# Kernel tuning notes

Measured on AMD Instinct MI355X. Metric: run time of the kernel, lower is better.

Reference implementation:

```python
import jax, jax.numpy as jnp
import numpy as np
from jax import lax

LOOKBACK = 336
N_FEATURES = 164
HORIZON = 96
D_MODEL = 64
D_STATE = 16
D_CONV = 4
EXPAND = 2
D_INNER = EXPAND * D_MODEL  # 128
DT_RANK = (D_MODEL + 15) // 16  # 4
MLP_HIDDEN = 64
BATCH = 512


def setup_inputs() -> dict:
    key = jax.random.key(0)
    ks = jax.random.split(key, 20)
    f32 = jnp.float32
    inp = {}
    inp["x_raw"] = jax.random.normal(ks[0], (BATCH, LOOKBACK), f32)
    inp["x_features"] = jax.random.normal(ks[1], (BATCH, N_FEATURES), f32)
    # embed Linear(1, d_model)
    inp["embed_W"] = jax.random.normal(ks[2], (1, D_MODEL), f32) * 0.5
    inp["embed_b"] = jnp.zeros((D_MODEL,), f32)
    # Mamba params (mamba-ssm layout, stored as [in, out] for matmul)
    inp["in_W"] = jax.random.normal(ks[3], (D_MODEL, 2 * D_INNER), f32) * (1.0 / np.sqrt(D_MODEL))
    inp["conv_W"] = jax.random.normal(ks[4], (D_INNER, D_CONV), f32) * 0.3
    inp["conv_b"] = jnp.zeros((D_INNER,), f32)
    inp["xproj_W"] = jax.random.normal(ks[5], (D_INNER, DT_RANK + 2 * D_STATE), f32) * (1.0 / np.sqrt(D_INNER))
    inp["dt_W"] = jax.random.normal(ks[6], (DT_RANK, D_INNER), f32) * (1.0 / np.sqrt(DT_RANK))
    inp["dt_b"] = jax.random.uniform(ks[7], (D_INNER,), f32, -4.0, -2.0)  # softplus -> small dt
    # A_log init = log(arange(1..d_state)) broadcast over d_inner, as in mamba-ssm
    inp["A_log"] = jnp.log(jnp.broadcast_to(jnp.arange(1, D_STATE + 1, dtype=f32), (D_INNER, D_STATE)))
    inp["D"] = jnp.ones((D_INNER,), f32)
    inp["out_W"] = jax.random.normal(ks[8], (D_INNER, D_MODEL), f32) * (1.0 / np.sqrt(D_INNER))
    # MLP stream
    inp["mlp_W1"] = jax.random.normal(ks[9], (N_FEATURES, MLP_HIDDEN), f32) * (1.0 / np.sqrt(N_FEATURES))
    inp["mlp_b1"] = jnp.zeros((MLP_HIDDEN,), f32)
    inp["mlp_W2"] = jax.random.normal(ks[10], (MLP_HIDDEN, MLP_HIDDEN // 2), f32) * (1.0 / np.sqrt(MLP_HIDDEN))
    inp["mlp_b2"] = jnp.zeros((MLP_HIDDEN // 2,), f32)
    # prediction head
    fin = D_MODEL + MLP_HIDDEN // 2
    inp["head_W"] = jax.random.normal(ks[11], (fin, HORIZON), f32) * (1.0 / np.sqrt(fin))
    inp["head_b"] = jnp.zeros((HORIZON,), f32)
    return inp


def silu(x):
    return x * jax.nn.sigmoid(x)


def mamba_block(u, in_W, conv_W, conv_b, xproj_W, dt_W, dt_b, A_log, D, out_W):
    # u: [B, L, d_model]
    B_, L, _ = u.shape
    xz = u @ in_W                      # [B, L, 2*D_INNER]
    x, z = jnp.split(xz, 2, axis=-1)   # each [B, L, D_INNER]
    # causal depthwise conv1d (pad left d_conv-1), then SiLU
    xc = x.transpose(0, 2, 1)          # [B, D_INNER, L]
    kern = conv_W[:, None, :]          # [D_INNER, 1, K] (OIH)
    xc = lax.conv_general_dilated(xc, kern, window_strides=(1,),
                                  padding=[(D_CONV - 1, 0)],
                                  dimension_numbers=("NCH", "OIH", "NCH"),
                                  feature_group_count=D_INNER)
    xc = silu(xc + conv_b[None, :, None])
    x = xc.transpose(0, 2, 1)          # [B, L, D_INNER]
    # input-dependent SSM params
    x_dbl = x @ xproj_W                # [B, L, DT_RANK + 2*D_STATE]
    dt = x_dbl[..., :DT_RANK]
    Bm = x_dbl[..., DT_RANK:DT_RANK + D_STATE]          # [B, L, N]
    Cm = x_dbl[..., DT_RANK + D_STATE:]                 # [B, L, N]
    delta = jax.nn.softplus(dt @ dt_W + dt_b)           # [B, L, D_INNER]
    A = -jnp.exp(A_log)                                 # [D_INNER, N]

    # selective scan over time
    def step(h, inps):
        d_t, B_t, C_t, x_t = inps  # [B,Di], [B,N], [B,N], [B,Di]
        dA = jnp.exp(d_t[:, :, None] * A[None])              # [B, Di, N]
        dBx = (d_t * x_t)[:, :, None] * B_t[:, None, :]      # [B, Di, N]
        h = dA * h + dBx
        y_t = jnp.einsum("bdn,bn->bd", h, C_t)
        return h, y_t

    h0 = jnp.zeros((B_, D_INNER, D_STATE), u.dtype)
    seq = (delta.transpose(1, 0, 2), Bm.transpose(1, 0, 2),
           Cm.transpose(1, 0, 2), x.transpose(1, 0, 2))
    _, ys = lax.scan(step, h0, seq)        # ys: [L, B, D_INNER]
    y = ys.transpose(1, 0, 2) + x * D[None, None, :]
    y = y * silu(z)
    return y @ out_W                        # [B, L, d_model]


def reference(x_raw, x_features, embed_W, embed_b, in_W, conv_W, conv_b,
              xproj_W, dt_W, dt_b, A_log, D, out_W,
              mlp_W1, mlp_b1, mlp_W2, mlp_b2, head_W, head_b):
    # embed raw series: [B, L] -> [B, L, 1] -> [B, L, d_model]
    h = x_raw[..., None] @ embed_W + embed_b
    h = mamba_block(h, in_W, conv_W, conv_b, xproj_W, dt_W, dt_b, A_log, D, out_W)
    h_mamba_out = h[:, -1, :]                       # [B, d_model]
    h_mlp = jax.nn.relu(x_features @ mlp_W1 + mlp_b1) @ mlp_W2 + mlp_b2
    h_final = jnp.concatenate([h_mamba_out, h_mlp], axis=1)
    return h_final @ head_W + head_b                # [B, horizon]
```

## Files before the change

kernel.cpp:

```cpp
#include <hip/hip_runtime.h>
#include <math.h>

#define LOOKBACK 336
#define NFEAT    164
#define HORIZON  96
#define DMODEL   64
#define DSTATE   16
#define DINNER   128
#define MLPH     64
#define BATCH    512
#define XCP      132
#define NG       4
#define GSEG     84
#define CHK      12
#define NCH      7
#define HSTR     20

typedef float v2f __attribute__((ext_vector_type(2)));

__device__ __forceinline__ float fast_rcp(float x) { return __builtin_amdgcn_rcpf(x); }
__device__ __forceinline__ float silu_f(float x) {
    return x * fast_rcp(1.f + __expf(-x));
}

__global__ __launch_bounds__(512, 2) void mamba_one(
    const float* __restrict__ x_raw,   const float* __restrict__ x_features,
    const float* __restrict__ embed_W, const float* __restrict__ embed_b,
    const float* __restrict__ in_W,
    const float* __restrict__ conv_W,  const float* __restrict__ conv_b,
    const float* __restrict__ xproj_W, const float* __restrict__ dt_W,
    const float* __restrict__ dt_b,    const float* __restrict__ A_log,
    const float* __restrict__ Dvec,    const float* __restrict__ out_W,
    const float* __restrict__ mlp_W1,  const float* __restrict__ mlp_b1,
    const float* __restrict__ mlp_W2,  const float* __restrict__ mlp_b2,
    const float* __restrict__ head_W,  const float* __restrict__ head_b,
    float* __restrict__ out)
{
    __shared__ __align__(16) float xrl[344];
    __shared__ __align__(16) float xprojT[20*XCP];
    __shared__ __align__(16) float xcbuf[2][NG][CHK*XCP];
    __shared__ __align__(16) float Bsh[NG][CHK][DSTATE];
    __shared__ __align__(16) float dtraw[NG][CHK][4];
    __shared__ float xcl[DINNER], zsil[DINNER], Cl[DSTATE], yv[DINNER];
    __shared__ float hfin[96], mlph[MLPH];

    const int tid = threadIdx.x;
    const int b   = blockIdx.x;
    const int g   = tid >> 7;
    const int ch  = tid & 127;

    for (int i = tid; i < 339; i += 512)
        xrl[i] = (i >= 3) ? x_raw[b*LOOKBACK + i - 3] : 0.f;
    for (int idx = tid; idx < 20*DINNER; idx += 512) {
        int jj = idx >> 7, d = idx & 127;
        xprojT[jj*XCP + d] = xproj_W[d*36 + jj];
    }

    float w1 = 0.f, w0 = 0.f;
    for (int dm = 0; dm < DMODEL; ++dm) {
        float w = in_W[dm*(2*DINNER) + ch];
        w1 = fmaf(embed_W[dm], w, w1);
        w0 = fmaf(embed_b[dm], w, w0);
    }
    const float4 cw = *(const float4*)&conv_W[ch*4];
    const float  cb = conv_b[ch];
    const float dtw0 = dt_W[ch],       dtw1 = dt_W[128 + ch],
                dtw2 = dt_W[256 + ch], dtw3 = dt_W[384 + ch];
    const float dtb_r = dt_b[ch];
    bool structured = true;
    #pragma unroll
    for (int i = 0; i < 16; ++i) {
        float a = __expf(A_log[ch*DSTATE + i]);
        float ex = (float)(i + 1);
        structured = structured && (fabsf(a - ex) < 1e-3f * ex);
    }
    const bool sfast = __all(structured);
    __syncthreads();

    {
        float* xw = &xcbuf[0][g][0];
        const float* xr = &xrl[g*GSEG];
        if (g == 0) {
            for (int tt = 0; tt < CHK; ++tt) {
                float acc = cb;
                if (tt >= 3) acc = fmaf(fmaf(xr[tt],   w1, w0), cw.x, acc);
                if (tt >= 2) acc = fmaf(fmaf(xr[tt+1], w1, w0), cw.y, acc);
                if (tt >= 1) acc = fmaf(fmaf(xr[tt+2], w1, w0), cw.z, acc);
                acc = fmaf(fmaf(xr[tt+3], w1, w0), cw.w, acc);
                xw[tt*XCP + ch] = silu_f(acc);
            }
        } else {
            float e0 = fmaf(xr[0], w1, w0);
            float e1 = fmaf(xr[1], w1, w0);
            float e2 = fmaf(xr[2], w1, w0);
            #pragma unroll
            for (int tt = 0; tt < CHK; ++tt) {
                float e3 = fmaf(xr[tt+3], w1, w0);
                float acc = cb + e0*cw.x + e1*cw.y + e2*cw.z + e3*cw.w;
                xw[tt*XCP + ch] = silu_f(acc);
                e0 = e1; e1 = e2; e2 = e3;
            }
        }
    }
    __syncthreads();

    v2f h01={0,0},h23={0,0},h45={0,0},h67={0,0},
        h89={0,0},hAB={0,0},hCD={0,0},hEF={0,0};
    float dacc = 0.f;

    for (int c = 0; c < NCH; ++c) {
        const int buf = c & 1;

        if (ch < 120) {
            const int tt = ch / 10;
            const int j0 = (ch - tt*10) * 2;
            const float* p0   = &xprojT[j0*XCP];
            const float* p1   = &xprojT[(j0+1)*XCP];
            const float* xrow = &xcbuf[buf][g][tt*XCP];
            v2f a0 = {0,0}, a1 = {0,0};
            #pragma unroll 8
            for (int d = 0; d < DINNER; d += 4) {
                float4 xv = *(const float4*)(xrow + d);
                float4 q0 = *(const float4*)(p0 + d);
                float4 q1 = *(const float4*)(p1 + d);
                v2f xl = {xv.x, xv.y}, xh = {xv.z, xv.w};
                v2f q0l = {q0.x, q0.y}, q0h = {q0.z, q0.w};
                v2f q1l = {q1.x, q1.y}, q1h = {q1.z, q1.w};
                a0 = __builtin_elementwise_fma(xl, q0l, a0);
                a0 = __builtin_elementwise_fma(xh, q0h, a0);
                a1 = __builtin_elementwise_fma(xl, q1l, a1);
                a1 = __builtin_elementwise_fma(xh, q1h, a1);
            }
            float r0 = a0.x + a0.y, r1 = a1.x + a1.y;
            if (j0 < 4) *(float2*)&dtraw[g][tt][j0] = make_float2(r0, r1);
            else        *(float2*)&Bsh[g][tt][j0-4] = make_float2(r0, r1);
        }
        __syncthreads();

        const float* xs = &xcbuf[buf][g][0];
        if (__builtin_expect(sfast, 1)) {
            #pragma unroll
            for (int tt = 0; tt < CHK; ++tt) {
                float4 dr = *(const float4*)&dtraw[g][tt][0];
                float dv = fmaf(dr.x, dtw0, fmaf(dr.y, dtw1,
                           fmaf(dr.z, dtw2, fmaf(dr.w, dtw3, dtb_r))));
                float e  = __expf(dv);
                float p  = 1.f + e;
                float r  = fast_rcp(p);
                float dl = (dv > 80.f) ? dv : __logf(p);
                dacc += dl;
                float ux = dl * xs[tt*XCP + ch];
                float4 B0 = *(const float4*)&Bsh[g][tt][0];
                float4 B1 = *(const float4*)&Bsh[g][tt][4];
                float4 B2 = *(const float4*)&Bsh[g][tt][8];
                float4 B3 = *(const float4*)&Bsh[g][tt][12];
                float r2 = r*r;
                v2f r2v = {r2, r2};
                v2f p01 = {r, r2};
                v2f p23 = p01*r2v, p45 = p23*r2v, p67 = p45*r2v, p89 = p67*r2v,
                    pAB = p89*r2v, pCD = pAB*r2v, pEF = pCD*r2v;
                v2f uxv = {ux, ux};
                h01 = __builtin_elementwise_fma(p01, h01, uxv*(v2f){B0.x,B0.y});
                h23 = __builtin_elementwise_fma(p23, h23, uxv*(v2f){B0.z,B0.w});
                h45 = __builtin_elementwise_fma(p45, h45, uxv*(v2f){B1.x,B1.y});
                h67 = __builtin_elementwise_fma(p67, h67, uxv*(v2f){B1.z,B1.w});
                h89 = __builtin_elementwise_fma(p89, h89, uxv*(v2f){B2.x,B2.y});
                hAB = __builtin_elementwise_fma(pAB, hAB, uxv*(v2f){B2.z,B2.w});
                hCD = __builtin_elementwise_fma(pCD, hCD, uxv*(v2f){B3.x,B3.y});
                hEF = __builtin_elementwise_fma(pEF, hEF, uxv*(v2f){B3.z,B3.w});
            }
        } else {
            const float* Arow = A_log + ch*DSTATE;
            for (int tt = 0; tt < CHK; ++tt) {
                float4 dr = *(const float4*)&dtraw[g][tt][0];
                float dv = fmaf(dr.x, dtw0, fmaf(dr.y, dtw1,
                           fmaf(dr.z, dtw2, fmaf(dr.w, dtw3, dtb_r))));
                float e  = __expf(dv);
                float dl = (dv > 15.f) ? dv : __logf(1.f + e);
                dacc += dl;
                float ux = dl * xs[tt*XCP + ch];
                const float* Brow = &Bsh[g][tt][0];
                float hv[16] = {h01.x,h01.y,h23.x,h23.y,h45.x,h45.y,h67.x,h67.y,
                                h89.x,h89.y,hAB.x,hAB.y,hCD.x,hCD.y,hEF.x,hEF.y};
                for (int i = 0; i < 16; ++i)
                    hv[i] = fmaf(__expf(-__expf(Arow[i])*dl), hv[i], ux*Brow[i]);
                h01=(v2f){hv[0],hv[1]};   h23=(v2f){hv[2],hv[3]};
                h45=(v2f){hv[4],hv[5]};   h67=(v2f){hv[6],hv[7]};
                h89=(v2f){hv[8],hv[9]};   hAB=(v2f){hv[10],hv[11]};
                hCD=(v2f){hv[12],hv[13]}; hEF=(v2f){hv[14],hv[15]};
            }
        }

        if (c + 1 < NCH) {
            float* xw = &xcbuf[buf^1][g][0];
            const float* xr = &xrl[g*GSEG + (c+1)*CHK];
            float e0 = fmaf(xr[0], w1, w0);
            float e1 = fmaf(xr[1], w1, w0);
            float e2 = fmaf(xr[2], w1, w0);
            float v = 0.f;
            #pragma unroll
            for (int tt = 0; tt < CHK; ++tt) {
                float e3 = fmaf(xr[tt+3], w1, w0);
                float acc = cb + e0*cw.x + e1*cw.y + e2*cw.z + e3*cw.w;
                v = silu_f(acc);
                xw[tt*XCP + ch] = v;
                e0 = e1; e1 = e2; e2 = e3;
            }
            if (g == NG-1 && c + 1 == NCH-1) xcl[ch] = v;
        }
        __syncthreads();
    }

    float* hpart = &xcbuf[0][0][0];
    float* dsum  = &Bsh[0][0][0];
    {
        float4* hp = (float4*)&hpart[(g*128 + ch)*HSTR];
        hp[0] = make_float4(h01.x,h01.y,h23.x,h23.y);
        hp[1] = make_float4(h45.x,h45.y,h67.x,h67.y);
        hp[2] = make_float4(h89.x,h89.y,hAB.x,hAB.y);
        hp[3] = make_float4(hCD.x,hCD.y,hEF.x,hEF.y);
        dsum[g*128 + ch] = dacc;
    }
    __syncthreads();

    float H[16];
    if (tid < 128) {
        {
            const float4* hp = (const float4*)&hpart[tid*HSTR];
            float4 a = hp[0], bq = hp[1], cq = hp[2], dq = hp[3];
            H[0]=a.x;  H[1]=a.y;  H[2]=a.z;  H[3]=a.w;
            H[4]=bq.x; H[5]=bq.y; H[6]=bq.z; H[7]=bq.w;
            H[8]=cq.x; H[9]=cq.y; H[10]=cq.z;H[11]=cq.w;
            H[12]=dq.x;H[13]=dq.y;H[14]=dq.z;H[15]=dq.w;
        }
        for (int gg = 1; gg < NG; ++gg) {
            float D = dsum[gg*128 + tid];
            const float4* hp = (const float4*)&hpart[(gg*128 + tid)*HSTR];
            float4 a = hp[0], bq = hp[1], cq = hp[2], dq = hp[3];
            float hg[16] = {a.x,a.y,a.z,a.w,bq.x,bq.y,bq.z,bq.w,
                            cq.x,cq.y,cq.z,cq.w,dq.x,dq.y,dq.z,dq.w};
            if (structured) {
                float r = __expf(-D);
                float pw = 1.f;
                #pragma unroll
                for (int i = 0; i < 16; ++i) {
                    pw *= r;
                    H[i] = fmaf(pw, H[i], hg[i]);
                }
            } else {
                #pragma unroll
                for (int i = 0; i < 16; ++i)
                    H[i] = fmaf(__expf(-__expf(A_log[tid*DSTATE+i])*D), H[i], hg[i]);
            }
        }
    } else if (tid < 256) {
        const int c2 = tid - 128;
        float a1 = 0.f, a0 = 0.f;
        for (int dm = 0; dm < DMODEL; ++dm) {
            float w = in_W[dm*(2*DINNER) + DINNER + c2];
            a1 = fmaf(embed_W[dm], w, a1);
            a0 = fmaf(embed_b[dm], w, a0);
        }
        float zv = fmaf(xrl[338], a1, a0);
        zsil[c2] = silu_f(zv);
    } else if (tid < 320) {
        const int lane = tid - 256;
        const int n = lane & 15, q = lane >> 4;
        float acc = 0.f;
        for (int d = q*32; d < q*32 + 32; ++d)
            acc = fmaf(xcl[d], xproj_W[d*36 + 20 + n], acc);
        acc += __shfl_xor(acc, 16);
        acc += __shfl_xor(acc, 32);
        if (lane < 16) Cl[n] = acc;
    } else if (tid >= 384) {
        const int lane = tid - 384;
        const int j = lane >> 1, k = lane & 1;
        const float* xf = x_features + b*NFEAT;
        float acc = 0.f;
        const int f0 = k*82, f1 = (k ? NFEAT : 82);
        for (int f = f0; f < f1; ++f)
            acc = fmaf(xf[f], mlp_W1[f*MLPH + j], acc);
        acc += __shfl_xor(acc, 1);
        if (k == 0) mlph[j] = fmaxf(acc + mlp_b1[j], 0.f);
    }
    __syncthreads();

    if (tid < 128) {
        float acc = 0.f;
        #pragma unroll
        for (int i = 0; i < 16; ++i) acc = fmaf(H[i], Cl[i], acc);
        float y = acc + xcl[tid]*Dvec[tid];
        yv[tid] = y * zsil[tid];
    } else if (tid < 192) {
        const int lane = tid - 128;
        const int j = lane >> 1, k = lane & 1;
        float acc = 0.f;
        for (int kk = k*32; kk < k*32 + 32; ++kk)
            acc = fmaf(mlph[kk], mlp_W2[kk*32 + j], acc);
        acc += __shfl_xor(acc, 1);
        if (k == 0) hfin[64 + j] = acc + mlp_b2[j];
    }
    __syncthreads();

    if (tid < 256) {
        const int o = tid >> 2, k = tid & 3;
        float acc = 0.f;
        for (int d = k*32; d < k*32 + 32; ++d)
            acc = fmaf(yv[d], out_W[d*DMODEL + o], acc);
        acc += __shfl_xor(acc, 1);
        acc += __shfl_xor(acc, 2);
        if (k == 0) hfin[o] = acc;
    }
    __syncthreads();

    if (tid < 192) {
        const int o = tid >> 1, k = tid & 1;
        float acc = 0.f;
        for (int i = k*48; i < k*48 + 48; ++i)
            acc = fmaf(hfin[i], head_W[i*HORIZON + o], acc);
        acc += __shfl_xor(acc, 1);
        if (k == 0) out[b*HORIZON + o] = acc + head_b[o];
    }
}

extern "C" void kernel_launch(void* const* d_in, const int* in_sizes, int n_in,
                              void* d_out, int out_size, void* d_ws, size_t ws_size,
                              hipStream_t stream) {
    (void)in_sizes; (void)n_in; (void)out_size; (void)d_ws; (void)ws_size;
    mamba_one<<<BATCH, 512, 0, stream>>>(
        (const float*)d_in[0],  (const float*)d_in[1],  (const float*)d_in[2],
        (const float*)d_in[3],  (const float*)d_in[4],  (const float*)d_in[5],
        (const float*)d_in[6],  (const float*)d_in[7],  (const float*)d_in[8],
        (const float*)d_in[9],  (const float*)d_in[10], (const float*)d_in[11],
        (const float*)d_in[12], (const float*)d_in[13], (const float*)d_in[14],
        (const float*)d_in[15], (const float*)d_in[16], (const float*)d_in[17],
        (const float*)d_in[18], (float*)d_out);
}
```

Measured before the change: 173.2 us.

## Precompute weight transposes and fused embed projections in a prep kernel

Adds a small prep kernel that writes the transposed xproj weights and the folded embed*in_W coefficients into workspace once per call, instead of every block recomputing them. The main kernel then reads the xproj columns from global/L2 rather than LDS, which removes that LDS array. Conv outputs are also kept in registers for the scan, which cuts LDS reads, and the thread-to-(timestep,column) mapping for the projection is rearranged. The cost is an extra kernel launch and global-memory loads in the inner dot-product loop instead of LDS loads.

```diff
diff --git a/kernel.cpp b/kernel.cpp
--- a/kernel.cpp
+++ b/kernel.cpp
@@ -16,11 +16,38 @@
 #define NCH      7
 #define HSTR     20
 
+#define XPJ      (20*DINNER)
+#define WSW1     XPJ
+#define WSW0     (XPJ + 2*DINNER)
+
 typedef float v2f __attribute__((ext_vector_type(2)));
 
 __device__ __forceinline__ float fast_rcp(float x) { return __builtin_amdgcn_rcpf(x); }
 __device__ __forceinline__ float silu_f(float x) {
     return x * fast_rcp(1.f + __expf(-x));
+}
+
+__global__ void prep_k(const float* __restrict__ xproj_W,
+                       const float* __restrict__ embed_W,
+                       const float* __restrict__ embed_b,
+                       const float* __restrict__ in_W,
+                       float* __restrict__ ws)
+{
+    const int idx = blockIdx.x * 512 + threadIdx.x;
+    if (idx < XPJ) {
+        const int j = idx >> 7, d = idx & 127;
+        ws[idx] = xproj_W[d * 36 + j];
+    } else if (idx < XPJ + 2 * DINNER) {
+        const int c = idx - XPJ;
+        float a1 = 0.f, a0 = 0.f;
+        for (int dm = 0; dm < DMODEL; ++dm) {
+            float w = in_W[dm * (2 * DINNER) + c];
+            a1 = fmaf(embed_W[dm], w, a1);
+            a0 = fmaf(embed_b[dm], w, a0);
+        }
+        ws[WSW1 + c] = a1;
+        ws[WSW0 + c] = a0;
+    }
 }
 
 __global__ __launch_bounds__(512, 2) void mamba_one(
@@ -34,10 +61,10 @@
     const float* __restrict__ mlp_W1,  const float* __restrict__ mlp_b1,
     const float* __restrict__ mlp_W2,  const float* __restrict__ mlp_b2,
     const float* __restrict__ head_W,  const float* __restrict__ head_b,
+    const float* __restrict__ ws,
     float* __restrict__ out)
 {
     __shared__ __align__(16) float xrl[344];
-    __shared__ __align__(16) float xprojT[20*XCP];
     __shared__ __align__(16) float xcbuf[2][NG][CHK*XCP];
     __shared__ __align__(16) float Bsh[NG][CHK][DSTATE];
     __shared__ __align__(16) float dtraw[NG][CHK][4];
@@ -49,19 +76,14 @@
     const int g   = tid >> 7;
     const int ch  = tid & 127;
 
+    const float* __restrict__ xpT = ws;
+    const float* __restrict__ pw1 = ws + WSW1;
+    const float* __restrict__ pw0 = ws + WSW0;
+
     for (int i = tid; i < 339; i += 512)
         xrl[i] = (i >= 3) ? x_raw[b*LOOKBACK + i - 3] : 0.f;
-    for (int idx = tid; idx < 20*DINNER; idx += 512) {
-        int jj = idx >> 7, d = idx & 127;
-        xprojT[jj*XCP + d] = xproj_W[d*36 + jj];
-    }
-
-    float w1 = 0.f, w0 = 0.f;
-    for (int dm = 0; dm < DMODEL; ++dm) {
-        float w = in_W[dm*(2*DINNER) + ch];
-        w1 = fmaf(embed_W[dm], w, w1);
-        w0 = fmaf(embed_b[dm], w, w0);
-    }
+
+    const float w1 = pw1[ch], w0 = pw0[ch];
     const float4 cw = *(const float4*)&conv_W[ch*4];
     const float  cb = conv_b[ch];
     const float dtw0 = dt_W[ch],       dtw1 = dt_W[128 + ch],
@@ -75,19 +97,29 @@
         structured = structured && (fabsf(a - ex) < 1e-3f * ex);
     }
     const bool sfast = __all(structured);
+
+    const int a2j0 = (ch / 12) * 2;
+    const int a2tt = ch % 12;
+    const float* __restrict__ a2p0 = xpT + a2j0 * DINNER;
+    const float* __restrict__ a2p1 = a2p0 + DINNER;
+
+    float xc_reg[CHK];
     __syncthreads();
 
     {
         float* xw = &xcbuf[0][g][0];
         const float* xr = &xrl[g*GSEG];
         if (g == 0) {
+            #pragma unroll
             for (int tt = 0; tt < CHK; ++tt) {
                 float acc = cb;
                 if (tt >= 3) acc = fmaf(fmaf(xr[tt],   w1, w0), cw.x, acc);
                 if (tt >= 2) acc = fmaf(fmaf(xr[tt+1], w1, w0), cw.y, acc);
                 if (tt >= 1) acc = fmaf(fmaf(xr[tt+2], w1, w0), cw.z, acc);
                 acc = fmaf(fmaf(xr[tt+3], w1, w0), cw.w, acc);
-                xw[tt*XCP + ch] = silu_f(acc);
+                float v = silu_f(acc);
+                xw[tt*XCP + ch] = v;
+                xc_reg[tt] = v;
             }
         } else {
             float e0 = fmaf(xr[0], w1, w0);
@@ -97,7 +129,9 @@
             for (int tt = 0; tt < CHK; ++tt) {
                 float e3 = fmaf(xr[tt+3], w1, w0);
                 float acc = cb + e0*cw.x + e1*cw.y + e2*cw.z + e3*cw.w;
-                xw[tt*XCP + ch] = silu_f(acc);
+                float v = silu_f(acc);
+                xw[tt*XCP + ch] = v;
+                xc_reg[tt] = v;
                 e0 = e1; e1 = e2; e2 = e3;
             }
         }
@@ -112,17 +146,13 @@
         const int buf = c & 1;
 
         if (ch < 120) {
-            const int tt = ch / 10;
-            const int j0 = (ch - tt*10) * 2;
-            const float* p0   = &xprojT[j0*XCP];
-            const float* p1   = &xprojT[(j0+1)*XCP];
-            const float* xrow = &xcbuf[buf][g][tt*XCP];
+            const float* xrow = &xcbuf[buf][g][a2tt*XCP];
             v2f a0 = {0,0}, a1 = {0,0};
             #pragma unroll 8
             for (int d = 0; d < DINNER; d += 4) {
                 float4 xv = *(const float4*)(xrow + d);
-                float4 q0 = *(const float4*)(p0 + d);
-                float4 q1 = *(const float4*)(p1 + d);
+                float4 q0 = *(const float4*)(a2p0 + d);
+                float4 q1 = *(const float4*)(a2p1 + d);
                 v2f xl = {xv.x, xv.y}, xh = {xv.z, xv.w};
                 v2f q0l = {q0.x, q0.y}, q0h = {q0.z, q0.w};
                 v2f q1l = {q1.x, q1.y}, q1h = {q1.z, q1.w};
@@ -132,12 +162,11 @@
                 a1 = __builtin_elementwise_fma(xh, q1h, a1);
             }
             float r0 = a0.x + a0.y, r1 = a1.x + a1.y;
-            if (j0 < 4) *(float2*)&dtraw[g][tt][j0] = make_float2(r0, r1);
-            else        *(float2*)&Bsh[g][tt][j0-4] = make_float2(r0, r1);
+            if (a2j0 < 4) *(float2*)&dtraw[g][a2tt][a2j0]   = make_float2(r0, r1);
+            else          *(float2*)&Bsh[g][a2tt][a2j0 - 4] = make_float2(r0, r1);
         }
         __syncthreads();
 
-        const float* xs = &xcbuf[buf][g][0];
         if (__builtin_expect(sfast, 1)) {
             #pragma unroll
             for (int tt = 0; tt < CHK; ++tt) {
@@ -149,7 +178,7 @@
                 float r  = fast_rcp(p);
                 float dl = (dv > 80.f) ? dv : __logf(p);
                 dacc += dl;
-                float ux = dl * xs[tt*XCP + ch];
+                float ux = dl * xc_reg[tt];
                 float4 B0 = *(const float4*)&Bsh[g][tt][0];
                 float4 B1 = *(const float4*)&Bsh[g][tt][4];
                 float4 B2 = *(const float4*)&Bsh[g][tt][8];
@@ -171,6 +200,7 @@
             }
         } else {
             const float* Arow = A_log + ch*DSTATE;
+            #pragma unroll
             for (int tt = 0; tt < CHK; ++tt) {
                 float4 dr = *(const float4*)&dtraw[g][tt][0];
                 float dv = fmaf(dr.x, dtw0, fmaf(dr.y, dtw1,
@@ -178,7 +208,7 @@
                 float e  = __expf(dv);
                 float dl = (dv > 15.f) ? dv : __logf(1.f + e);
                 dacc += dl;
-                float ux = dl * xs[tt*XCP + ch];
+                float ux = dl * xc_reg[tt];
                 const float* Brow = &Bsh[g][tt][0];
                 float hv[16] = {h01.x,h01.y,h23.x,h23.y,h45.x,h45.y,h67.x,h67.y,
                                 h89.x,h89.y,hAB.x,hAB.y,hCD.x,hCD.y,hEF.x,hEF.y};
@@ -204,6 +234,7 @@
                 float acc = cb + e0*cw.x + e1*cw.y + e2*cw.z + e3*cw.w;
                 v = silu_f(acc);
                 xw[tt*XCP + ch] = v;
+                xc_reg[tt] = v;
                 e0 = e1; e1 = e2; e2 = e3;
             }
             if (g == NG-1 && c + 1 == NCH-1) xcl[ch] = v;
@@ -255,13 +286,7 @@
         }
     } else if (tid < 256) {
         const int c2 = tid - 128;
-        float a1 = 0.f, a0 = 0.f;
-        for (int dm = 0; dm < DMODEL; ++dm) {
-            float w = in_W[dm*(2*DINNER) + DINNER + c2];
-            a1 = fmaf(embed_W[dm], w, a1);
-            a0 = fmaf(embed_b[dm], w, a0);
-        }
-        float zv = fmaf(xrl[338], a1, a0);
+        float zv = fmaf(xrl[338], pw1[DINNER + c2], pw0[DINNER + c2]);
         zsil[c2] = silu_f(zv);
     } else if (tid < 320) {
         const int lane = tid - 256;
@@ -326,7 +351,11 @@
 extern "C" void kernel_launch(void* const* d_in, const int* in_sizes, int n_in,
                               void* d_out, int out_size, void* d_ws, size_t ws_size,
                               hipStream_t stream) {
-    (void)in_sizes; (void)n_in; (void)out_size; (void)d_ws; (void)ws_size;
+    (void)in_sizes; (void)n_in; (void)out_size; (void)ws_size;
+    float* ws = (float*)d_ws;
+    prep_k<<<6, 512, 0, stream>>>((const float*)d_in[7],  (const float*)d_in[2],
+                                  (const float*)d_in[3],  (const float*)d_in[4],
+                                  ws);
     mamba_one<<<BATCH, 512, 0, stream>>>(
         (const float*)d_in[0],  (const float*)d_in[1],  (const float*)d_in[2],
         (const float*)d_in[3],  (const float*)d_in[4],  (const float*)d_in[5],
@@ -334,5 +363,5 @@
         (const float*)d_in[9],  (const float*)d_in[10], (const float*)d_in[11],
         (const float*)d_in[12], (const float*)d_in[13], (const float*)d_in[14],
         (const float*)d_in[15], (const float*)d_in[16], (const float*)d_in[17],
-        (const float*)d_in[18], (float*)d_out);
+        (const float*)d_in[18], ws, (float*)d_out);
 }
```

New measurement: 232.3 us. 1.34x slower.

## Split each batch's sequence scan across four 128-thread blocks with global-memory combine

Applied to the files above, without the earlier changes.

Each batch was one 512-thread block holding four sequence segments. It is now four 128-thread blocks, one per segment. Segments 0-2 write their partial SSM state and delta sums to a workspace and signal an atomic counter. The last segment's block spins until that counter reaches 3, then combines the states and runs the epilogue. The aim is finer-grained scheduling and less shared memory per block, with register-held conv outputs replacing double-buffered shared rows. The trade-offs are a memset launch, global-memory round trips, and a spin-wait that can deadlock if the dependent blocks are not co-resident or scheduled.

```diff
diff --git a/kernel.cpp b/kernel.cpp
--- a/kernel.cpp
+++ b/kernel.cpp
@@ -10,11 +10,13 @@
 #define MLPH     64
 #define BATCH    512
 #define XCP      132
-#define NG       4
 #define GSEG     84
 #define CHK      12
 #define NCH      7
-#define HSTR     20
+
+#define WS_H     512
+#define WS_D     (WS_H + BATCH*3*DINNER*DSTATE)
+#define WS_FLOATS (WS_D + BATCH*3*DINNER)
 
 typedef float v2f __attribute__((ext_vector_type(2)));
 
@@ -23,7 +25,7 @@
     return x * fast_rcp(1.f + __expf(-x));
 }
 
-__global__ __launch_bounds__(512, 2) void mamba_one(
+__global__ __launch_bounds__(128, 4) void mamba_seg(
     const float* __restrict__ x_raw,   const float* __restrict__ x_features,
     const float* __restrict__ embed_W, const float* __restrict__ embed_b,
     const float* __restrict__ in_W,
@@ -34,26 +36,27 @@
     const float* __restrict__ mlp_W1,  const float* __restrict__ mlp_b1,
     const float* __restrict__ mlp_W2,  const float* __restrict__ mlp_b2,
     const float* __restrict__ head_W,  const float* __restrict__ head_b,
-    float* __restrict__ out)
+    float* __restrict__ ws,            float* __restrict__ out)
 {
-    __shared__ __align__(16) float xrl[344];
+    __shared__ __align__(16) float xr[88];
     __shared__ __align__(16) float xprojT[20*XCP];
-    __shared__ __align__(16) float xcbuf[2][NG][CHK*XCP];
-    __shared__ __align__(16) float Bsh[NG][CHK][DSTATE];
-    __shared__ __align__(16) float dtraw[NG][CHK][4];
-    __shared__ float xcl[DINNER], zsil[DINNER], Cl[DSTATE], yv[DINNER];
-    __shared__ float hfin[96], mlph[MLPH];
-
-    const int tid = threadIdx.x;
-    const int b   = blockIdx.x;
-    const int g   = tid >> 7;
-    const int ch  = tid & 127;
-
-    for (int i = tid; i < 339; i += 512)
-        xrl[i] = (i >= 3) ? x_raw[b*LOOKBACK + i - 3] : 0.f;
-    for (int idx = tid; idx < 20*DINNER; idx += 512) {
-        int jj = idx >> 7, d = idx & 127;
-        xprojT[jj*XCP + d] = xproj_W[d*36 + jj];
+    __shared__ __align__(16) float xcbuf[CHK*XCP];
+    __shared__ __align__(16) float Bsh[CHK][DSTATE];
+    __shared__ __align__(16) float dtraw[CHK][4];
+    __shared__ __align__(16) float xcl[DINNER];
+
+    const int tid   = threadIdx.x;
+    const int batch = blockIdx.x >> 2;
+    const int g     = blockIdx.x & 3;
+    const int ch    = tid;
+
+    for (int i = tid; i < 87; i += 128) {
+        int t = g*GSEG - 3 + i;
+        xr[i] = (t >= 0) ? x_raw[batch*LOOKBACK + t] : 0.f;
+    }
+    for (int idx = tid; idx < 20*DINNER; idx += 128) {
+        int j = idx >> 7, d = idx & 127;
+        xprojT[j*XCP + d] = xproj_W[d*36 + j];
     }
 
     float w1 = 0.f, w0 = 0.f;
@@ -75,29 +78,35 @@
         structured = structured && (fabsf(a - ex) < 1e-3f * ex);
     }
     const bool sfast = __all(structured);
-    __syncthreads();
-
-    {
-        float* xw = &xcbuf[0][g][0];
-        const float* xr = &xrl[g*GSEG];
+
+    float xc_reg[CHK];
+    __syncthreads();
+
+    {
+        const float* xp = xr;
         if (g == 0) {
+            #pragma unroll
             for (int tt = 0; tt < CHK; ++tt) {
                 float acc = cb;
-                if (tt >= 3) acc = fmaf(fmaf(xr[tt],   w1, w0), cw.x, acc);
-                if (tt >= 2) acc = fmaf(fmaf(xr[tt+1], w1, w0), cw.y, acc);
-                if (tt >= 1) acc = fmaf(fmaf(xr[tt+2], w1, w0), cw.z, acc);
-                acc = fmaf(fmaf(xr[tt+3], w1, w0), cw.w, acc);
-                xw[tt*XCP + ch] = silu_f(acc);
+                if (tt >= 3) acc = fmaf(fmaf(xp[tt],   w1, w0), cw.x, acc);
+                if (tt >= 2) acc = fmaf(fmaf(xp[tt+1], w1, w0), cw.y, acc);
+                if (tt >= 1) acc = fmaf(fmaf(xp[tt+2], w1, w0), cw.z, acc);
+                acc = fmaf(fmaf(xp[tt+3], w1, w0), cw.w, acc);
+                float v = silu_f(acc);
+                xcbuf[tt*XCP + ch] = v;
+                xc_reg[tt] = v;
             }
         } else {
-            float e0 = fmaf(xr[0], w1, w0);
-            float e1 = fmaf(xr[1], w1, w0);
-            float e2 = fmaf(xr[2], w1, w0);
-            #pragma unroll
-            for (int tt = 0; tt < CHK; ++tt) {
-                float e3 = fmaf(xr[tt+3], w1, w0);
+            float e0 = fmaf(xp[0], w1, w0);
+            float e1 = fmaf(xp[1], w1, w0);
+            float e2 = fmaf(xp[2], w1, w0);
+            #pragma unroll
+            for (int tt = 0; tt < CHK; ++tt) {
+                float e3 = fmaf(xp[tt+3], w1, w0);
                 float acc = cb + e0*cw.x + e1*cw.y + e2*cw.z + e3*cw.w;
-                xw[tt*XCP + ch] = silu_f(acc);
+                float v = silu_f(acc);
+                xcbuf[tt*XCP + ch] = v;
+                xc_reg[tt] = v;
                 e0 = e1; e1 = e2; e2 = e3;
             }
         }
@@ -109,14 +118,12 @@
     float dacc = 0.f;
 
     for (int c = 0; c < NCH; ++c) {
-        const int buf = c & 1;
-
         if (ch < 120) {
             const int tt = ch / 10;
             const int j0 = (ch - tt*10) * 2;
             const float* p0   = &xprojT[j0*XCP];
             const float* p1   = &xprojT[(j0+1)*XCP];
-            const float* xrow = &xcbuf[buf][g][tt*XCP];
+            const float* xrow = &xcbuf[tt*XCP];
             v2f a0 = {0,0}, a1 = {0,0};
             #pragma unroll 8
             for (int d = 0; d < DINNER; d += 4) {
@@ -132,16 +139,15 @@
                 a1 = __builtin_elementwise_fma(xh, q1h, a1);
             }
             float r0 = a0.x + a0.y, r1 = a1.x + a1.y;
-            if (j0 < 4) *(float2*)&dtraw[g][tt][j0] = make_float2(r0, r1);
-            else        *(float2*)&Bsh[g][tt][j0-4] = make_float2(r0, r1);
+            if (j0 < 4) *(float2*)&dtraw[tt][j0]   = make_float2(r0, r1);
+            else        *(float2*)&Bsh[tt][j0 - 4] = make_float2(r0, r1);
         }
         __syncthreads();
 
-        const float* xs = &xcbuf[buf][g][0];
         if (__builtin_expect(sfast, 1)) {
             #pragma unroll
             for (int tt = 0; tt < CHK; ++tt) {
-                float4 dr = *(const float4*)&dtraw[g][tt][0];
+                float4 dr = *(const float4*)&dtraw[tt][0];
                 float dv = fmaf(dr.x, dtw0, fmaf(dr.y, dtw1,
                            fmaf(dr.z, dtw2, fmaf(dr.w, dtw3, dtb_r))));
                 float e  = __expf(dv);
@@ -149,11 +155,11 @@
                 float r  = fast_rcp(p);
                 float dl = (dv > 80.f) ? dv : __logf(p);
                 dacc += dl;
-                float ux = dl * xs[tt*XCP + ch];
-                float4 B0 = *(const float4*)&Bsh[g][tt][0];
-                float4 B1 = *(const float4*)&Bsh[g][tt][4];
-                float4 B2 = *(const float4*)&Bsh[g][tt][8];
-                float4 B3 = *(const float4*)&Bsh[g][tt][12];
+                float ux = dl * xc_reg[tt];
+                float4 B0 = *(const float4*)&Bsh[tt][0];
+                float4 B1 = *(const float4*)&Bsh[tt][4];
+                float4 B2 = *(const float4*)&Bsh[tt][8];
+                float4 B3 = *(const float4*)&Bsh[tt][12];
                 float r2 = r*r;
                 v2f r2v = {r2, r2};
                 v2f p01 = {r, r2};
@@ -171,15 +177,16 @@
             }
         } else {
             const float* Arow = A_log + ch*DSTATE;
-            for (int tt = 0; tt < CHK; ++tt) {
-                float4 dr = *(const float4*)&dtraw[g][tt][0];
+            #pragma unroll
+            for (int tt = 0; tt < CHK; ++tt) {
+                float4 dr = *(const float4*)&dtraw[tt][0];
                 float dv = fmaf(dr.x, dtw0, fmaf(dr.y, dtw1,
                            fmaf(dr.z, dtw2, fmaf(dr.w, dtw3, dtb_r))));
                 float e  = __expf(dv);
                 float dl = (dv > 15.f) ? dv : __logf(1.f + e);
                 dacc += dl;
-                float ux = dl * xs[tt*XCP + ch];
-                const float* Brow = &Bsh[g][tt][0];
+                float ux = dl * xc_reg[tt];
+                const float* Brow = &Bsh[tt][0];
                 float hv[16] = {h01.x,h01.y,h23.x,h23.y,h45.x,h45.y,h67.x,h67.y,
                                 h89.x,h89.y,hAB.x,hAB.y,hCD.x,hCD.y,hEF.x,hEF.y};
                 for (int i = 0; i < 16; ++i)
@@ -192,90 +199,143 @@
         }
 
         if (c + 1 < NCH) {
-            float* xw = &xcbuf[buf^1][g][0];
-            const float* xr = &xrl[g*GSEG + (c+1)*CHK];
-            float e0 = fmaf(xr[0], w1, w0);
-            float e1 = fmaf(xr[1], w1, w0);
-            float e2 = fmaf(xr[2], w1, w0);
+            const float* xp = &xr[(c+1)*CHK];
+            float e0 = fmaf(xp[0], w1, w0);
+            float e1 = fmaf(xp[1], w1, w0);
+            float e2 = fmaf(xp[2], w1, w0);
             float v = 0.f;
             #pragma unroll
             for (int tt = 0; tt < CHK; ++tt) {
-                float e3 = fmaf(xr[tt+3], w1, w0);
+                float e3 = fmaf(xp[tt+3], w1, w0);
                 float acc = cb + e0*cw.x + e1*cw.y + e2*cw.z + e3*cw.w;
                 v = silu_f(acc);
-                xw[tt*XCP + ch] = v;
+                xcbuf[tt*XCP + ch] = v;
+                xc_reg[tt] = v;
                 e0 = e1; e1 = e2; e2 = e3;
             }
-            if (g == NG-1 && c + 1 == NCH-1) xcl[ch] = v;
+            if (g == 3 && c + 1 == NCH-1) xcl[ch] = v;
         }
         __syncthreads();
     }
 
-    float* hpart = &xcbuf[0][0][0];
-    float* dsum  = &Bsh[0][0][0];
-    {
-        float4* hp = (float4*)&hpart[(g*128 + ch)*HSTR];
-        hp[0] = make_float4(h01.x,h01.y,h23.x,h23.y);
-        hp[1] = make_float4(h45.x,h45.y,h67.x,h67.y);
-        hp[2] = make_float4(h89.x,h89.y,hAB.x,hAB.y);
-        hp[3] = make_float4(hCD.x,hCD.y,hEF.x,hEF.y);
-        dsum[g*128 + ch] = dacc;
-    }
-    __syncthreads();
+    if (g < 3) {
+        float* hw = ws + WS_H + (size_t)((batch*3 + g)*DINNER + ch)*DSTATE;
+        float4* h4 = (float4*)hw;
+        h4[0] = make_float4(h01.x,h01.y,h23.x,h23.y);
+        h4[1] = make_float4(h45.x,h45.y,h67.x,h67.y);
+        h4[2] = make_float4(h89.x,h89.y,hAB.x,hAB.y);
+        h4[3] = make_float4(hCD.x,hCD.y,hEF.x,hEF.y);
+        ws[WS_D + (batch*3 + g)*DINNER + ch] = dacc;
+        __threadfence();
+        __syncthreads();
+        if (tid == 0)
+            __hip_atomic_fetch_add((int*)ws + batch, 1,
+                                   __ATOMIC_RELEASE, __HIP_MEMORY_SCOPE_AGENT);
+        return;
+    }
+
+    if (tid == 0) {
+        while (__hip_atomic_load((int*)ws + batch,
+                                 __ATOMIC_ACQUIRE, __HIP_MEMORY_SCOPE_AGENT) < 3)
+            __builtin_amdgcn_s_sleep(16);
+    }
+    __syncthreads();
+    __threadfence();
 
     float H[16];
-    if (tid < 128) {
-        {
-            const float4* hp = (const float4*)&hpart[tid*HSTR];
+    {
+        const float4* hp = (const float4*)(ws + WS_H + (size_t)((batch*3)*DINNER + ch)*DSTATE);
+        float4 a = hp[0], bq = hp[1], cq = hp[2], dq = hp[3];
+        H[0]=a.x;  H[1]=a.y;  H[2]=a.z;  H[3]=a.w;
+        H[4]=bq.x; H[5]=bq.y; H[6]=bq.z; H[7]=bq.w;
+        H[8]=cq.x; H[9]=cq.y; H[10]=cq.z;H[11]=cq.w;
+        H[12]=dq.x;H[13]=dq.y;H[14]=dq.z;H[15]=dq.w;
+    }
+    for (int gg = 1; gg <= 3; ++gg) {
+        float Dg;
+        float hg[16];
+        if (gg < 3) {
+            Dg = ws[WS_D + (batch*3 + gg)*DINNER + ch];
+            const float4* hp = (const float4*)(ws + WS_H + (size_t)((batch*3 + gg)*DINNER + ch)*DSTATE);
             float4 a = hp[0], bq = hp[1], cq = hp[2], dq = hp[3];
-            H[0]=a.x;  H[1]=a.y;  H[2]=a.z;  H[3]=a.w;
-            H[4]=bq.x; H[5]=bq.y; H[6]=bq.z; H[7]=bq.w;
-            H[8]=cq.x; H[9]=cq.y; H[10]=cq.z;H[11]=cq.w;
-            H[12]=dq.x;H[13]=dq.y;H[14]=dq.z;H[15]=dq.w;
-        }
-        for (int gg = 1; gg < NG; ++gg) {
-            float D = dsum[gg*128 + tid];
-            const float4* hp = (const float4*)&hpart[(gg*128 + tid)*HSTR];
-            float4 a = hp[0], bq = hp[1], cq = hp[2], dq = hp[3];
-            float hg[16] = {a.x,a.y,a.z,a.w,bq.x,bq.y,bq.z,bq.w,
-                            cq.x,cq.y,cq.z,cq.w,dq.x,dq.y,dq.z,dq.w};
-            if (structured) {
-                float r = __expf(-D);
-                float pw = 1.f;
-                #pragma unroll
-                for (int i = 0; i < 16; ++i) {
-                    pw *= r;
-                    H[i] = fmaf(pw, H[i], hg[i]);
-                }
-            } else {
-                #pragma unroll
-                for (int i = 0; i < 16; ++i)
-                    H[i] = fmaf(__expf(-__expf(A_log[tid*DSTATE+i])*D), H[i], hg[i]);
-            }
-        }
-    } else if (tid < 256) {
-        const int c2 = tid - 128;
+            hg[0]=a.x;  hg[1]=a.y;  hg[2]=a.z;  hg[3]=a.w;
+            hg[4]=bq.x; hg[5]=bq.y; hg[6]=bq.z; hg[7]=bq.w;
+            hg[8]=cq.x; hg[9]=cq.y; hg[10]=cq.z;hg[11]=cq.w;
+            hg[12]=dq.x;hg[13]=dq.y;hg[14]=dq.z;hg[15]=dq.w;
+        } else {
+            Dg = dacc;
+            hg[0]=h01.x; hg[1]=h01.y; hg[2]=h23.x; hg[3]=h23.y;
+            hg[4]=h45.x; hg[5]=h45.y; hg[6]=h67.x; hg[7]=h67.y;
+            hg[8]=h89.x; hg[9]=h89.y; hg[10]=hAB.x;hg[11]=hAB.y;
+            hg[12]=hCD.x;hg[13]=hCD.y;hg[14]=hEF.x;hg[15]=hEF.y;
+        }
+        if (structured) {
+            float r = __expf(-Dg);
+            float pw = 1.f;
+            #pragma unroll
+            for (int i = 0; i < 16; ++i) {
+                pw *= r;
+                H[i] = fmaf(pw, H[i], hg[i]);
+            }
+        } else {
+            #pragma unroll
+            for (int i = 0; i < 16; ++i)
+                H[i] = fmaf(__expf(-__expf(A_log[ch*DSTATE+i])*Dg), H[i], hg[i]);
+        }
+    }
+
+    float* Cpart = xcbuf;
+    float* hfin  = xcbuf + 32;
+    float* mlph  = xcbuf + 128;
+    float* yvs   = xcbuf + 192;
+
+    float zs;
+    {
         float a1 = 0.f, a0 = 0.f;
         for (int dm = 0; dm < DMODEL; ++dm) {
-            float w = in_W[dm*(2*DINNER) + DINNER + c2];
+            float w = in_W[dm*(2*DINNER) + DINNER + ch];
             a1 = fmaf(embed_W[dm], w, a1);
             a0 = fmaf(embed_b[dm], w, a0);
         }
-        float zv = fmaf(xrl[338], a1, a0);
-        zsil[c2] = silu_f(zv);
-    } else if (tid < 320) {
-        const int lane = tid - 256;
-        const int n = lane & 15, q = lane >> 4;
-        float acc = 0.f;
-        for (int d = q*32; d < q*32 + 32; ++d)
+        zs = silu_f(fmaf(xr[86], a1, a0));
+    }
+
+    {
+        const int lw = ch & 63, wv = ch >> 6;
+        const int n = lw & 15, q = lw >> 4;
+        const int d0 = wv*64 + q*16;
+        float acc = 0.f;
+        for (int dd = 0; dd < 16; ++dd) {
+            int d = d0 + dd;
             acc = fmaf(xcl[d], xproj_W[d*36 + 20 + n], acc);
+        }
         acc += __shfl_xor(acc, 16);
         acc += __shfl_xor(acc, 32);
-        if (lane < 16) Cl[n] = acc;
-    } else if (tid >= 384) {
-        const int lane = tid - 384;
-        const int j = lane >> 1, k = lane & 1;
-        const float* xf = x_features + b*NFEAT;
+        if (lw < 16) Cpart[wv*16 + n] = acc;
+    }
+    __syncthreads();
+
+    {
+        float acc = 0.f;
+        #pragma unroll
+        for (int i = 0; i < 16; ++i)
+            acc = fmaf(H[i], Cpart[i] + Cpart[16 + i], acc);
+        float y = acc + xcl[ch]*Dvec[ch];
+        yvs[ch] = y * zs;
+    }
+    __syncthreads();
+
+    {
+        const int o = ch >> 1, k = ch & 1;
+        float acc = 0.f;
+        for (int d = k*64; d < k*64 + 64; ++d)
+            acc = fmaf(yvs[d], out_W[d*DMODEL + o], acc);
+        acc += __shfl_xor(acc, 1);
+        if (k == 0) hfin[o] = acc;
+    }
+    {
+        const int j = ch >> 1, k = ch & 1;
+        const float* xf = x_features + batch*NFEAT;
         float acc = 0.f;
         const int f0 = k*82, f1 = (k ? NFEAT : 82);
         for (int f = f0; f < f1; ++f)
@@ -285,15 +345,8 @@
     }
     __syncthreads();
 
-    if (tid < 128) {
-        float acc = 0.f;
-        #pragma unroll
-        for (int i = 0; i < 16; ++i) acc = fmaf(H[i], Cl[i], acc);
-        float y = acc + xcl[tid]*Dvec[tid];
-        yv[tid] = y * zsil[tid];
-    } else if (tid < 192) {
-        const int lane = tid - 128;
-        const int j = lane >> 1, k = lane & 1;
+    if (ch < 64) {
+        const int j = ch >> 1, k = ch & 1;
         float acc = 0.f;
         for (int kk = k*32; kk < k*32 + 32; ++kk)
             acc = fmaf(mlph[kk], mlp_W2[kk*32 + j], acc);
@@ -302,37 +355,25 @@
     }
     __syncthreads();
 
-    if (tid < 256) {
-        const int o = tid >> 2, k = tid & 3;
-        float acc = 0.f;
-        for (int d = k*32; d < k*32 + 32; ++d)
-            acc = fmaf(yv[d], out_W[d*DMODEL + o], acc);
-        acc += __shfl_xor(acc, 1);
-        acc += __shfl_xor(acc, 2);
-        if (k == 0) hfin[o] = acc;
-    }
-    __syncthreads();
-
-    if (tid < 192) {
-        const int o = tid >> 1, k = tid & 1;
-        float acc = 0.f;
-        for (int i = k*48; i < k*48 + 48; ++i)
-            acc = fmaf(hfin[i], head_W[i*HORIZON + o], acc);
-        acc += __shfl_xor(acc, 1);
-        if (k == 0) out[b*HORIZON + o] = acc + head_b[o];
+    if (ch < HORIZON) {
+        float acc = 0.f;
+        for (int i = 0; i < 96; ++i)
+            acc = fmaf(hfin[i], head_W[i*HORIZON + ch], acc);
+        out[batch*HORIZON + ch] = acc + head_b[ch];
     }
 }
 
 extern "C" void kernel_launch(void* const* d_in, const int* in_sizes, int n_in,
                               void* d_out, int out_size, void* d_ws, size_t ws_size,
                               hipStream_t stream) {
-    (void)in_sizes; (void)n_in; (void)out_size; (void)d_ws; (void)ws_size;
-    mamba_one<<<BATCH, 512, 0, stream>>>(
+    (void)in_sizes; (void)n_in; (void)out_size; (void)ws_size;
+    hipMemsetAsync(d_ws, 0, BATCH*sizeof(int), stream);
+    mamba_seg<<<BATCH*4, 128, 0, stream>>>(
         (const float*)d_in[0],  (const float*)d_in[1],  (const float*)d_in[2],
         (const float*)d_in[3],  (const float*)d_in[4],  (const float*)d_in[5],
         (const float*)d_in[6],  (const float*)d_in[7],  (const float*)d_in[8],
         (const float*)d_in[9],  (const float*)d_in[10], (const float*)d_in[11],
         (const float*)d_in[12], (const float*)d_in[13], (const float*)d_in[14],
         (const float*)d_in[15], (const float*)d_in[16], (const float*)d_in[17],
-        (const float*)d_in[18], (float*)d_out);
+        (const float*)d_in[18], (float*)d_ws, (float*)d_out);
 }
```

Result: slower. 411.0 us (+137.3%).

## Single-buffer conv output in LDS, cache it in registers, raise occupancy hint

Applied to the files above, without the earlier changes.

Replaces the double-buffered conv-output LDS array with one shared buffer. Each thread keeps its own conv outputs in a register array, so the scan reads them from registers instead of LDS. The end-of-scan partial-state exchange moves to a strided float4 layout that reuses the smaller buffer. The launch-bounds occupancy hint goes from 2 to 6, which makes more resident work possible through lower LDS use but also caps registers and risks spills.

```diff
diff --git a/kernel.cpp b/kernel.cpp
--- a/kernel.cpp
+++ b/kernel.cpp
@@ -14,7 +14,6 @@
 #define GSEG     84
 #define CHK      12
 #define NCH      7
-#define HSTR     20
 
 typedef float v2f __attribute__((ext_vector_type(2)));
 
@@ -23,7 +22,7 @@
     return x * fast_rcp(1.f + __expf(-x));
 }
 
-__global__ __launch_bounds__(512, 2) void mamba_one(
+__global__ __launch_bounds__(512, 6) void mamba_one(
     const float* __restrict__ x_raw,   const float* __restrict__ x_features,
     const float* __restrict__ embed_W, const float* __restrict__ embed_b,
     const float* __restrict__ in_W,
@@ -38,7 +37,7 @@
 {
     __shared__ __align__(16) float xrl[344];
     __shared__ __align__(16) float xprojT[20*XCP];
-    __shared__ __align__(16) float xcbuf[2][NG][CHK*XCP];
+    __shared__ __align__(16) float xcu[8192];
     __shared__ __align__(16) float Bsh[NG][CHK][DSTATE];
     __shared__ __align__(16) float dtraw[NG][CHK][4];
     __shared__ float xcl[DINNER], zsil[DINNER], Cl[DSTATE], yv[DINNER];
@@ -75,19 +74,24 @@
         structured = structured && (fabsf(a - ex) < 1e-3f * ex);
     }
     const bool sfast = __all(structured);
+
+    float xc_reg[CHK];
+    float* const xcg = &xcu[g*(CHK*XCP)];
     __syncthreads();
 
     {
-        float* xw = &xcbuf[0][g][0];
         const float* xr = &xrl[g*GSEG];
         if (g == 0) {
+            #pragma unroll
             for (int tt = 0; tt < CHK; ++tt) {
                 float acc = cb;
                 if (tt >= 3) acc = fmaf(fmaf(xr[tt],   w1, w0), cw.x, acc);
                 if (tt >= 2) acc = fmaf(fmaf(xr[tt+1], w1, w0), cw.y, acc);
                 if (tt >= 1) acc = fmaf(fmaf(xr[tt+2], w1, w0), cw.z, acc);
                 acc = fmaf(fmaf(xr[tt+3], w1, w0), cw.w, acc);
-                xw[tt*XCP + ch] = silu_f(acc);
+                float v = silu_f(acc);
+                xcg[tt*XCP + ch] = v;
+                xc_reg[tt] = v;
             }
         } else {
             float e0 = fmaf(xr[0], w1, w0);
@@ -97,7 +101,9 @@
             for (int tt = 0; tt < CHK; ++tt) {
                 float e3 = fmaf(xr[tt+3], w1, w0);
                 float acc = cb + e0*cw.x + e1*cw.y + e2*cw.z + e3*cw.w;
-                xw[tt*XCP + ch] = silu_f(acc);
+                float v = silu_f(acc);
+                xcg[tt*XCP + ch] = v;
+                xc_reg[tt] = v;
                 e0 = e1; e1 = e2; e2 = e3;
             }
         }
@@ -109,14 +115,12 @@
     float dacc = 0.f;
 
     for (int c = 0; c < NCH; ++c) {
-        const int buf = c & 1;
-
         if (ch < 120) {
             const int tt = ch / 10;
             const int j0 = (ch - tt*10) * 2;
             const float* p0   = &xprojT[j0*XCP];
             const float* p1   = &xprojT[(j0+1)*XCP];
-            const float* xrow = &xcbuf[buf][g][tt*XCP];
+            const float* xrow = &xcg[tt*XCP];
             v2f a0 = {0,0}, a1 = {0,0};
             #pragma unroll 8
             for (int d = 0; d < DINNER; d += 4) {
@@ -137,7 +141,6 @@
         }
         __syncthreads();
 
-        const float* xs = &xcbuf[buf][g][0];
         if (__builtin_expect(sfast, 1)) {
             #pragma unroll
             for (int tt = 0; tt < CHK; ++tt) {
@@ -149,7 +152,7 @@
                 float r  = fast_rcp(p);
                 float dl = (dv > 80.f) ? dv : __logf(p);
                 dacc += dl;
-                float ux = dl * xs[tt*XCP + ch];
+                float ux = dl * xc_reg[tt];
                 float4 B0 = *(const float4*)&Bsh[g][tt][0];
                 float4 B1 = *(const float4*)&Bsh[g][tt][4];
                 float4 B2 = *(const float4*)&Bsh[g][tt][8];
@@ -171,6 +174,7 @@
             }
         } else {
             const float* Arow = A_log + ch*DSTATE;
+            #pragma unroll
             for (int tt = 0; tt < CHK; ++tt) {
                 float4 dr = *(const float4*)&dtraw[g][tt][0];
                 float dv = fmaf(dr.x, dtw0, fmaf(dr.y, dtw1,
@@ -178,7 +182,7 @@
                 float e  = __expf(dv);
                 float dl = (dv > 15.f) ? dv : __logf(1.f + e);
                 dacc += dl;
-                float ux = dl * xs[tt*XCP + ch];
+                float ux = dl * xc_reg[tt];
                 const float* Brow = &Bsh[g][tt][0];
                 float hv[16] = {h01.x,h01.y,h23.x,h23.y,h45.x,h45.y,h67.x,h67.y,
                                 h89.x,h89.y,hAB.x,hAB.y,hCD.x,hCD.y,hEF.x,hEF.y};
@@ -192,7 +196,6 @@
         }
 
         if (c + 1 < NCH) {
-            float* xw = &xcbuf[buf^1][g][0];
             const float* xr = &xrl[g*GSEG + (c+1)*CHK];
             float e0 = fmaf(xr[0], w1, w0);
             float e1 = fmaf(xr[1], w1, w0);
@@ -203,7 +206,8 @@
                 float e3 = fmaf(xr[tt+3], w1, w0);
                 float acc = cb + e0*cw.x + e1*cw.y + e2*cw.z + e3*cw.w;
                 v = silu_f(acc);
-                xw[tt*XCP + ch] = v;
+                xcg[tt*XCP + ch] = v;
+                xc_reg[tt] = v;
                 e0 = e1; e1 = e2; e2 = e3;
             }
             if (g == NG-1 && c + 1 == NCH-1) xcl[ch] = v;
@@ -211,23 +215,23 @@
         __syncthreads();
     }
 
-    float* hpart = &xcbuf[0][0][0];
-    float* dsum  = &Bsh[0][0][0];
+    float4* const hp4 = (float4*)xcu;
+    float*  const dsum = &Bsh[0][0][0];
     {
-        float4* hp = (float4*)&hpart[(g*128 + ch)*HSTR];
-        hp[0] = make_float4(h01.x,h01.y,h23.x,h23.y);
-        hp[1] = make_float4(h45.x,h45.y,h67.x,h67.y);
-        hp[2] = make_float4(h89.x,h89.y,hAB.x,hAB.y);
-        hp[3] = make_float4(hCD.x,hCD.y,hEF.x,hEF.y);
-        dsum[g*128 + ch] = dacc;
+        const int idx = g*128 + ch;
+        hp4[0*512 + idx] = make_float4(h01.x,h01.y,h23.x,h23.y);
+        hp4[1*512 + idx] = make_float4(h45.x,h45.y,h67.x,h67.y);
+        hp4[2*512 + idx] = make_float4(h89.x,h89.y,hAB.x,hAB.y);
+        hp4[3*512 + idx] = make_float4(hCD.x,hCD.y,hEF.x,hEF.y);
+        dsum[idx] = dacc;
     }
     __syncthreads();
 
     float H[16];
     if (tid < 128) {
         {
-            const float4* hp = (const float4*)&hpart[tid*HSTR];
-            float4 a = hp[0], bq = hp[1], cq = hp[2], dq = hp[3];
+            float4 a  = hp4[0*512 + tid], bq = hp4[1*512 + tid];
+            float4 cq = hp4[2*512 + tid], dq = hp4[3*512 + tid];
             H[0]=a.x;  H[1]=a.y;  H[2]=a.z;  H[3]=a.w;
             H[4]=bq.x; H[5]=bq.y; H[6]=bq.z; H[7]=bq.w;
             H[8]=cq.x; H[9]=cq.y; H[10]=cq.z;H[11]=cq.w;
@@ -235,8 +239,8 @@
         }
         for (int gg = 1; gg < NG; ++gg) {
             float D = dsum[gg*128 + tid];
-            const float4* hp = (const float4*)&hpart[(gg*128 + tid)*HSTR];
-            float4 a = hp[0], bq = hp[1], cq = hp[2], dq = hp[3];
+            float4 a  = hp4[0*512 + gg*128 + tid], bq = hp4[1*512 + gg*128 + tid];
+            float4 cq = hp4[2*512 + gg*128 + tid], dq = hp4[3*512 + gg*128 + tid];
             float hg[16] = {a.x,a.y,a.z,a.w,bq.x,bq.y,bq.z,bq.w,
                             cq.x,cq.y,cq.z,cq.w,dq.x,dq.y,dq.z,dq.w};
             if (structured) {
```

New measurement: 199.9 us. 15.4% more time.
